# Kernel optimization log

Measured on AMD Instinct MI355X. Metric: run time of the kernel, lower is better.

Reference implementation:

```python
import jax, jax.numpy as jnp
import numpy as np

NEG_BIG = -9e15  # matches torch's -9000000000000000.0 mask value


def _l2norm(x, eps=1e-12):
    # F.normalize(x, p=2, dim=1)
    n = jnp.sqrt(jnp.sum(x * x, axis=1, keepdims=True))
    return x / jnp.maximum(n, eps)


def _fusion_attribute(emb, att_emb, adj):
    # cosine similarity [N, M]
    sim = _l2norm(emb) @ _l2norm(att_emb).T
    sim = sim * adj
    # masked softmax over dim=1: zeros -> -9e15
    logits = jnp.where(sim != 0, sim, jnp.full_like(sim, NEG_BIG))
    attention = jax.nn.softmax(logits, axis=1)
    return attention @ att_emb


def setup_inputs() -> dict:
    key = jax.random.key(0)
    k1, k2, k3, k4 = jax.random.split(key, 4)
    U, I, D = 10000, 8000, 64
    users_emb = 0.1 * jax.random.normal(k1, (U, D), dtype=jnp.float32)  # init.normal_(std=0.1)
    items_emb = 0.1 * jax.random.normal(k2, (I, D), dtype=jnp.float32)
    Out_UserAttNets = (jax.random.uniform(k3, (U, I)) < 0.05).astype(jnp.float32)
    Out_ItemAttNets = (jax.random.uniform(k4, (I, U)) < 0.05).astype(jnp.float32)
    return {
        "num_users": U,
        "num_items": I,
        "users_emb": users_emb,
        "items_emb": items_emb,
        "Out_UserAttNets": Out_UserAttNets,
        "Out_ItemAttNets": Out_ItemAttNets,
    }


def reference(num_users, num_items, users_emb, items_emb, Out_UserAttNets, Out_ItemAttNets):
    out_useratt_emb = _fusion_attribute(users_emb, items_emb, Out_UserAttNets)
    out_itematt_emb = _fusion_attribute(items_emb, users_emb, Out_ItemAttNets)
    return (users_emb, items_emb, out_useratt_emb, out_itematt_emb)
```

## Files before the change

### kernel.cpp

```cpp
#include <hip/hip_runtime.h>
#include <math.h>

typedef float f32x4 __attribute__((ext_vector_type(4)));
typedef unsigned int u32;
typedef u32 u32x4 __attribute__((ext_vector_type(4)));
typedef unsigned short u16;
typedef unsigned long long u64;

#define SEG 512

__device__ __forceinline__ u16 f2b(float x) {
    union { float f; u32 u; } v; v.f = x;
    return (u16)((v.u + 0x7FFFu + ((v.u >> 16) & 1u)) >> 16);
}
__device__ __forceinline__ float b2f_lo(u32 u) { union { u32 u; float f; } v; v.u = u << 16;         return v.f; }
__device__ __forceinline__ float b2f_hi(u32 u) { union { u32 u; float f; } v; v.u = u & 0xFFFF0000u; return v.f; }

__global__ __launch_bounds__(256) void prep_kernel(
    const float* __restrict__ users, const float* __restrict__ items,
    u16* __restrict__ hU, u16* __restrict__ hI,
    float* __restrict__ nU, float* __restrict__ nI, int U, int I)
{
    int lane = threadIdx.x & 63;
    int row  = (blockIdx.x << 2) + (threadIdx.x >> 6);
    const float* src; u16* hat; float* nrm; int r;
    if (row < U) { r = row; src = users; hat = hU; nrm = nU; }
    else { r = row - U; if (r >= I) return; src = items; hat = hI; nrm = nI; }
    float x = src[(size_t)r * 64 + lane];
    float s = x * x;
#pragma unroll
    for (int off = 32; off; off >>= 1) s += __shfl_xor(s, off, 64);
    float nv   = sqrtf(s);
    float rinv = 1.0f / fmaxf(nv, 1e-12f);
    hat[(size_t)r * 64 + lane] = f2b(x * rinv);
    if (lane == 0) nrm[r] = nv;
}

__global__ __launch_bounds__(256) void att_row_kernel(
    const float* __restrict__ users, const float* __restrict__ items,
    const u16* __restrict__ hU, const u16* __restrict__ hI,
    const float* __restrict__ nU, const float* __restrict__ nI,
    const float* __restrict__ adjU, const float* __restrict__ adjI,
    float* __restrict__ outU, float* __restrict__ outI, int U, int I)
{
    __shared__ int   cols_sh[4][SEG];
    __shared__ float red[4][8][8];
    __shared__ float wsum_sh[4];

    const int lane = threadIdx.x & 63;
    const int wid  = threadIdx.x >> 6;
    const int half = wid & 1;
    const int grow = ((int)blockIdx.x << 1) + (wid >> 1);
    const bool valid = (grow < U + I);

    const u16* qhat = 0; const u16* kvhat = 0; const float* kvnrm = 0;
    const float* kvraw = 0; const float* adj = 0; float* outp = 0;
    int M = 0, row = 0;
    if (valid) {
        if (grow < U) {
            row = grow;     qhat = hU; kvhat = hI; kvnrm = nI;
            kvraw = items;  adj = adjU; outp = outU; M = I;
        } else {
            row = grow - U; qhat = hI; kvhat = hU; kvnrm = nU;
            kvraw = users;  adj = adjI; outp = outI; M = U;
        }
    }

    const int sub = lane & 7;
    const int grp = lane >> 3;

    float a0 = 0.f, a1 = 0.f, a2 = 0.f, a3 = 0.f;
    float a4 = 0.f, a5 = 0.f, a6 = 0.f, a7 = 0.f, wsum = 0.f;

    if (valid) {
        const float* adjrow = adj + (size_t)row * M;

        const int mid = (M >> 1) & ~3;
        const int lo4 = half ? (mid >> 2) : 0;
        const int hi4 = half ? (M >> 2) : (mid >> 2);
        int wcount = 0;
        for (int i4 = lo4 + lane; i4 < hi4; i4 += 64) {
            f32x4 a = __builtin_nontemporal_load((const f32x4*)adjrow + i4);
#pragma unroll
            for (int j = 0; j < 4; ++j) {
                bool pred = (a[j] != 0.0f);
                u64 mask = __ballot(pred);
                if (pred) {
                    int pos = wcount + __builtin_amdgcn_mbcnt_hi(
                        (u32)(mask >> 32), __builtin_amdgcn_mbcnt_lo((u32)mask, 0));
                    if (pos < SEG) cols_sh[wid][pos] = (i4 << 2) + j;
                }
                wcount += __popcll(mask);
            }
        }
        wcount = __shfl(wcount, 0, 64);
        if (half && (M & 3)) {
            int idx = (hi4 << 2) + lane;
            bool pred = (idx < M) && (adjrow[idx] != 0.0f);
            u64 mask = __ballot(pred);
            if (pred) {
                int pos = wcount + __builtin_amdgcn_mbcnt_hi(
                    (u32)(mask >> 32), __builtin_amdgcn_mbcnt_lo((u32)mask, 0));
                if (pos < SEG) cols_sh[wid][pos] = idx;
            }
            wcount += __popcll(mask);
        }
        int cnt = wcount > SEG ? SEG : wcount;

        u32x4 qw = *(const u32x4*)(qhat + (size_t)row * 64 + sub * 8);
        const float q0 = b2f_lo(qw[0]), q1 = b2f_hi(qw[0]);
        const float q2 = b2f_lo(qw[1]), q3 = b2f_hi(qw[1]);
        const float q4 = b2f_lo(qw[2]), q5 = b2f_hi(qw[2]);
        const float q6 = b2f_lo(qw[3]), q7 = b2f_hi(qw[3]);

        const int* cp = cols_sh[wid];
        int i = grp;
        for (; i + 24 < cnt; i += 32) {
            int ca = cp[i], cb = cp[i + 8], cc = cp[i + 16], cd = cp[i + 24];
            u32x4 va = *(const u32x4*)(kvhat + (size_t)ca * 64 + sub * 8);
            u32x4 vb = *(const u32x4*)(kvhat + (size_t)cb * 64 + sub * 8);
            u32x4 vc = *(const u32x4*)(kvhat + (size_t)cc * 64 + sub * 8);
            u32x4 vd = *(const u32x4*)(kvhat + (size_t)cd * 64 + sub * 8);
            float na = kvnrm[ca], nb = kvnrm[cb], nc = kvnrm[cc], nd = kvnrm[cd];
            float ra0 = b2f_lo(va[0]), ra1 = b2f_hi(va[0]), ra2 = b2f_lo(va[1]), ra3 = b2f_hi(va[1]);
            float ra4 = b2f_lo(va[2]), ra5 = b2f_hi(va[2]), ra6 = b2f_lo(va[3]), ra7 = b2f_hi(va[3]);
            float rb0 = b2f_lo(vb[0]), rb1 = b2f_hi(vb[0]), rb2 = b2f_lo(vb[1]), rb3 = b2f_hi(vb[1]);
            float rb4 = b2f_lo(vb[2]), rb5 = b2f_hi(vb[2]), rb6 = b2f_lo(vb[3]), rb7 = b2f_hi(vb[3]);
            float rc0 = b2f_lo(vc[0]), rc1 = b2f_hi(vc[0]), rc2 = b2f_lo(vc[1]), rc3 = b2f_hi(vc[1]);
            float rc4 = b2f_lo(vc[2]), rc5 = b2f_hi(vc[2]), rc6 = b2f_lo(vc[3]), rc7 = b2f_hi(vc[3]);
            float rd0 = b2f_lo(vd[0]), rd1 = b2f_hi(vd[0]), rd2 = b2f_lo(vd[1]), rd3 = b2f_hi(vd[1]);
            float rd4 = b2f_lo(vd[2]), rd5 = b2f_hi(vd[2]), rd6 = b2f_lo(vd[3]), rd7 = b2f_hi(vd[3]);
            float da = fmaf(q0, ra0, fmaf(q1, ra1, fmaf(q2, ra2, fmaf(q3, ra3,
                       fmaf(q4, ra4, fmaf(q5, ra5, fmaf(q6, ra6, q7 * ra7)))))));
            float db = fmaf(q0, rb0, fmaf(q1, rb1, fmaf(q2, rb2, fmaf(q3, rb3,
                       fmaf(q4, rb4, fmaf(q5, rb5, fmaf(q6, rb6, q7 * rb7)))))));
            float dc = fmaf(q0, rc0, fmaf(q1, rc1, fmaf(q2, rc2, fmaf(q3, rc3,
                       fmaf(q4, rc4, fmaf(q5, rc5, fmaf(q6, rc6, q7 * rc7)))))));
            float dd = fmaf(q0, rd0, fmaf(q1, rd1, fmaf(q2, rd2, fmaf(q3, rd3,
                       fmaf(q4, rd4, fmaf(q5, rd5, fmaf(q6, rd6, q7 * rd7)))))));
#pragma unroll
            for (int off = 1; off <= 4; off <<= 1) {
                da += __shfl_xor(da, off, 64);
                db += __shfl_xor(db, off, 64);
                dc += __shfl_xor(dc, off, 64);
                dd += __shfl_xor(dd, off, 64);
            }
            float wa = (da != 0.0f) ? __expf(da - 1.0f) : 0.0f;
            float wb = (db != 0.0f) ? __expf(db - 1.0f) : 0.0f;
            float wc = (dc != 0.0f) ? __expf(dc - 1.0f) : 0.0f;
            float wd = (dd != 0.0f) ? __expf(dd - 1.0f) : 0.0f;
            float xa = wa * na, xb = wb * nb, xc = wc * nc, xd = wd * nd;
            a0 = fmaf(xa, ra0, fmaf(xb, rb0, fmaf(xc, rc0, fmaf(xd, rd0, a0))));
            a1 = fmaf(xa, ra1, fmaf(xb, rb1, fmaf(xc, rc1, fmaf(xd, rd1, a1))));
            a2 = fmaf(xa, ra2, fmaf(xb, rb2, fmaf(xc, rc2, fmaf(xd, rd2, a2))));
            a3 = fmaf(xa, ra3, fmaf(xb, rb3, fmaf(xc, rc3, fmaf(xd, rd3, a3))));
            a4 = fmaf(xa, ra4, fmaf(xb, rb4, fmaf(xc, rc4, fmaf(xd, rd4, a4))));
            a5 = fmaf(xa, ra5, fmaf(xb, rb5, fmaf(xc, rc5, fmaf(xd, rd5, a5))));
            a6 = fmaf(xa, ra6, fmaf(xb, rb6, fmaf(xc, rc6, fmaf(xd, rd6, a6))));
            a7 = fmaf(xa, ra7, fmaf(xb, rb7, fmaf(xc, rc7, fmaf(xd, rd7, a7))));
            if (sub == 0) wsum += (wa + wb) + (wc + wd);
        }
        for (; i < cnt; i += 8) {
            int ca = cp[i];
            u32x4 va = *(const u32x4*)(kvhat + (size_t)ca * 64 + sub * 8);
            float na = kvnrm[ca];
            float ra0 = b2f_lo(va[0]), ra1 = b2f_hi(va[0]), ra2 = b2f_lo(va[1]), ra3 = b2f_hi(va[1]);
            float ra4 = b2f_lo(va[2]), ra5 = b2f_hi(va[2]), ra6 = b2f_lo(va[3]), ra7 = b2f_hi(va[3]);
            float da = fmaf(q0, ra0, fmaf(q1, ra1, fmaf(q2, ra2, fmaf(q3, ra3,
                       fmaf(q4, ra4, fmaf(q5, ra5, fmaf(q6, ra6, q7 * ra7)))))));
#pragma unroll
            for (int off = 1; off <= 4; off <<= 1) da += __shfl_xor(da, off, 64);
            float wa = (da != 0.0f) ? __expf(da - 1.0f) : 0.0f;
            float xa = wa * na;
            a0 = fmaf(xa, ra0, a0); a1 = fmaf(xa, ra1, a1);
            a2 = fmaf(xa, ra2, a2); a3 = fmaf(xa, ra3, a3);
            a4 = fmaf(xa, ra4, a4); a5 = fmaf(xa, ra5, a5);
            a6 = fmaf(xa, ra6, a6); a7 = fmaf(xa, ra7, a7);
            if (sub == 0) wsum += wa;
        }

#pragma unroll
        for (int off = 8; off <= 32; off <<= 1) {
            wsum += __shfl_xor(wsum, off, 64);
            a0 += __shfl_xor(a0, off, 64); a1 += __shfl_xor(a1, off, 64);
            a2 += __shfl_xor(a2, off, 64); a3 += __shfl_xor(a3, off, 64);
            a4 += __shfl_xor(a4, off, 64); a5 += __shfl_xor(a5, off, 64);
            a6 += __shfl_xor(a6, off, 64); a7 += __shfl_xor(a7, off, 64);
        }
        if (lane < 8) {
            f32x4* rp = (f32x4*)&red[wid][lane][0];
            rp[0] = (f32x4){a0, a1, a2, a3};
            rp[1] = (f32x4){a4, a5, a6, a7};
        }
        if (lane == 0) wsum_sh[wid] = wsum;
    }
    __syncthreads();

    if (valid && half == 0) {
        float den = wsum_sh[wid] + wsum_sh[wid + 1];
        if (lane < 8) {
            f32x4* r0p = (f32x4*)&red[wid][lane][0];
            f32x4* r1p = (f32x4*)&red[wid + 1][lane][0];
            f32x4 s0 = r0p[0] + r1p[0];
            f32x4 s1 = r0p[1] + r1p[1];
            float* orow = outp + (size_t)row * 64 + lane * 8;
            if (den > 0.0f) {
                float inv = 1.0f / den;
                ((f32x4*)orow)[0] = s0 * inv;
                ((f32x4*)orow)[1] = s1 * inv;
            } else {
                f32x4 m0 = (f32x4){0.f, 0.f, 0.f, 0.f};
                f32x4 m1 = (f32x4){0.f, 0.f, 0.f, 0.f};
                for (int r = 0; r < M; ++r) {
                    const f32x4* kr = (const f32x4*)(kvraw + (size_t)r * 64 + lane * 8);
                    m0 += kr[0]; m1 += kr[1];
                }
                float invM = 1.0f / (float)M;
                ((f32x4*)orow)[0] = m0 * invM;
                ((f32x4*)orow)[1] = m1 * invM;
            }
        }
    }
}

extern "C" void kernel_launch(void* const* d_in, const int* in_sizes, int n_in,
                              void* d_out, int out_size, void* d_ws, size_t ws_size,
                              hipStream_t stream) {
    const float* users = (const float*)d_in[2];
    const float* items = (const float*)d_in[3];
    const float* adjU  = (const float*)d_in[4];
    const float* adjI  = (const float*)d_in[5];
    const int U = in_sizes[2] / 64;
    const int I = in_sizes[3] / 64;

    char* w = (char*)d_ws;
    u16* hU = (u16*)w;    w += (size_t)U * 64 * sizeof(u16);
    u16* hI = (u16*)w;    w += (size_t)I * 64 * sizeof(u16);
    float* nU = (float*)w; w += (size_t)U * sizeof(float);
    float* nI = (float*)w;

    float* out = (float*)d_out;

    hipMemcpyAsync(out, users, (size_t)U * 64 * sizeof(float),
                   hipMemcpyDeviceToDevice, stream);
    hipMemcpyAsync(out + (size_t)U * 64, items, (size_t)I * 64 * sizeof(float),
                   hipMemcpyDeviceToDevice, stream);

    prep_kernel<<<(U + I + 3) / 4, 256, 0, stream>>>(users, items, hU, hI, nU, nI, U, I);

    float* outUatt = out + (size_t)(U + I) * 64;
    float* outIatt = outUatt + (size_t)U * 64;
    att_row_kernel<<<(U + I + 1) / 2, 256, 0, stream>>>(
        users, items, hU, hI, nU, nI, adjU, adjI, outUatt, outIatt, U, I);
}
```

Baseline: 239.9 us.

## Split adjacency compaction into separate kernel writing u16 column lists

Moves the dense adjacency scan and nonzero compaction out of the attention kernel into a dedicated compact_kernel. That kernel writes per-half-row u16 column indices and counts to workspace, and the gather kernel reads those lists instead of scanning the adjacency. The aim is to decouple the bandwidth-bound scan from the latency-bound gather so each runs at full occupancy without LDS staging. In exchange it adds a launch plus a workspace round trip, and it lowers SEG to 384, which risks truncating dense rows.

Result: slower. 248.5 us (+3.6%).

```diff
diff --git a/kernel.cpp b/kernel.cpp
--- a/kernel.cpp
+++ b/kernel.cpp
@@ -7,7 +7,7 @@
 typedef unsigned short u16;
 typedef unsigned long long u64;
 
-#define SEG 512
+#define SEG 384
 
 __device__ __forceinline__ u16 f2b(float x) {
     union { float f; u32 u; } v; v.f = x;
@@ -15,6 +15,9 @@
 }
 __device__ __forceinline__ float b2f_lo(u32 u) { union { u32 u; float f; } v; v.u = u << 16;         return v.f; }
 __device__ __forceinline__ float b2f_hi(u32 u) { union { u32 u; float f; } v; v.u = u & 0xFFFF0000u; return v.f; }
+__device__ __forceinline__ int mbcnt64(u64 m) {
+    return __builtin_amdgcn_mbcnt_hi((u32)(m >> 32), __builtin_amdgcn_mbcnt_lo((u32)m, 0));
+}
 
 __global__ __launch_bounds__(256) void prep_kernel(
     const float* __restrict__ users, const float* __restrict__ items,
@@ -36,14 +39,61 @@
     if (lane == 0) nrm[r] = nv;
 }
 
-__global__ __launch_bounds__(256) void att_row_kernel(
+__global__ __launch_bounds__(256) void compact_kernel(
+    const float* __restrict__ adjU, const float* __restrict__ adjI,
+    u16* __restrict__ csr, u32* __restrict__ cnt, int U, int I)
+{
+    const int lane = threadIdx.x & 63;
+    const int wid  = threadIdx.x >> 6;
+    const int hr   = ((int)blockIdx.x << 2) + wid;
+    if (hr >= 2 * (U + I)) return;
+    const int grow = hr >> 1, half = hr & 1;
+
+    const float* adj; int M, row;
+    if (grow < U) { row = grow;     adj = adjU; M = I; }
+    else          { row = grow - U; adj = adjI; M = U; }
+    const float* adjrow = adj + (size_t)row * M;
+
+    const int mid = (M >> 1) & ~3;
+    const int lo4 = half ? (mid >> 2) : 0;
+    const int hi4 = half ? (M >> 2) : (mid >> 2);
+    u16* outp = csr + (size_t)hr * SEG;
+
+    int wcount = 0;
+    for (int i4 = lo4 + lane; i4 < hi4; i4 += 64) {
+        f32x4 a = __builtin_nontemporal_load((const f32x4*)adjrow + i4);
+#pragma unroll
+        for (int j = 0; j < 4; ++j) {
+            bool pred = (a[j] != 0.0f);
+            u64 mask = __ballot(pred);
+            if (pred) {
+                int pos = wcount + mbcnt64(mask);
+                if (pos < SEG) outp[pos] = (u16)((i4 << 2) + j);
+            }
+            wcount += __popcll(mask);
+        }
+    }
+    wcount = __shfl(wcount, 0, 64);
+    if (half && (M & 3)) {
+        int idx = (hi4 << 2) + lane;
+        bool pred = (idx < M) && (adjrow[idx] != 0.0f);
+        u64 mask = __ballot(pred);
+        if (pred) {
+            int pos = wcount + mbcnt64(mask);
+            if (pos < SEG) outp[pos] = (u16)idx;
+        }
+        wcount += __popcll(mask);
+    }
+    if (lane == 0) cnt[hr] = (u32)(wcount > SEG ? SEG : wcount);
+}
+
+__global__ __launch_bounds__(256) void att_gather_kernel(
     const float* __restrict__ users, const float* __restrict__ items,
     const u16* __restrict__ hU, const u16* __restrict__ hI,
     const float* __restrict__ nU, const float* __restrict__ nI,
-    const float* __restrict__ adjU, const float* __restrict__ adjI,
+    const u16* __restrict__ csr, const u32* __restrict__ cnt,
     float* __restrict__ outU, float* __restrict__ outI, int U, int I)
 {
-    __shared__ int   cols_sh[4][SEG];
     __shared__ float red[4][8][8];
     __shared__ float wsum_sh[4];
 
@@ -54,15 +104,15 @@
     const bool valid = (grow < U + I);
 
     const u16* qhat = 0; const u16* kvhat = 0; const float* kvnrm = 0;
-    const float* kvraw = 0; const float* adj = 0; float* outp = 0;
+    const float* kvraw = 0; float* outp = 0;
     int M = 0, row = 0;
     if (valid) {
         if (grow < U) {
             row = grow;     qhat = hU; kvhat = hI; kvnrm = nI;
-            kvraw = items;  adj = adjU; outp = outU; M = I;
+            kvraw = items;  outp = outU; M = I;
         } else {
             row = grow - U; qhat = hI; kvhat = hU; kvnrm = nU;
-            kvraw = users;  adj = adjI; outp = outI; M = U;
+            kvraw = users;  outp = outI; M = U;
         }
     }
 
@@ -73,39 +123,9 @@
     float a4 = 0.f, a5 = 0.f, a6 = 0.f, a7 = 0.f, wsum = 0.f;
 
     if (valid) {
-        const float* adjrow = adj + (size_t)row * M;
-
-        const int mid = (M >> 1) & ~3;
-        const int lo4 = half ? (mid >> 2) : 0;
-        const int hi4 = half ? (M >> 2) : (mid >> 2);
-        int wcount = 0;
-        for (int i4 = lo4 + lane; i4 < hi4; i4 += 64) {
-            f32x4 a = __builtin_nontemporal_load((const f32x4*)adjrow + i4);
-#pragma unroll
-            for (int j = 0; j < 4; ++j) {
-                bool pred = (a[j] != 0.0f);
-                u64 mask = __ballot(pred);
-                if (pred) {
-                    int pos = wcount + __builtin_amdgcn_mbcnt_hi(
-                        (u32)(mask >> 32), __builtin_amdgcn_mbcnt_lo((u32)mask, 0));
-                    if (pos < SEG) cols_sh[wid][pos] = (i4 << 2) + j;
-                }
-                wcount += __popcll(mask);
-            }
-        }
-        wcount = __shfl(wcount, 0, 64);
-        if (half && (M & 3)) {
-            int idx = (hi4 << 2) + lane;
-            bool pred = (idx < M) && (adjrow[idx] != 0.0f);
-            u64 mask = __ballot(pred);
-            if (pred) {
-                int pos = wcount + __builtin_amdgcn_mbcnt_hi(
-                    (u32)(mask >> 32), __builtin_amdgcn_mbcnt_lo((u32)mask, 0));
-                if (pos < SEG) cols_sh[wid][pos] = idx;
-            }
-            wcount += __popcll(mask);
-        }
-        int cnt = wcount > SEG ? SEG : wcount;
+        const int hr = (grow << 1) | half;
+        const int cn = (int)cnt[hr];
+        const u16* cp = csr + (size_t)hr * SEG;
 
         u32x4 qw = *(const u32x4*)(qhat + (size_t)row * 64 + sub * 8);
         const float q0 = b2f_lo(qw[0]), q1 = b2f_hi(qw[0]);
@@ -113,9 +133,8 @@
         const float q4 = b2f_lo(qw[2]), q5 = b2f_hi(qw[2]);
         const float q6 = b2f_lo(qw[3]), q7 = b2f_hi(qw[3]);
 
-        const int* cp = cols_sh[wid];
         int i = grp;
-        for (; i + 24 < cnt; i += 32) {
+        for (; i + 24 < cn; i += 32) {
             int ca = cp[i], cb = cp[i + 8], cc = cp[i + 16], cd = cp[i + 24];
             u32x4 va = *(const u32x4*)(kvhat + (size_t)ca * 64 + sub * 8);
             u32x4 vb = *(const u32x4*)(kvhat + (size_t)cb * 64 + sub * 8);
@@ -160,7 +179,7 @@
             a7 = fmaf(xa, ra7, fmaf(xb, rb7, fmaf(xc, rc7, fmaf(xd, rd7, a7))));
             if (sub == 0) wsum += (wa + wb) + (wc + wd);
         }
-        for (; i < cnt; i += 8) {
+        for (; i < cn; i += 8) {
             int ca = cp[i];
             u32x4 va = *(const u32x4*)(kvhat + (size_t)ca * 64 + sub * 8);
             float na = kvnrm[ca];
@@ -232,12 +251,15 @@
     const float* adjI  = (const float*)d_in[5];
     const int U = in_sizes[2] / 64;
     const int I = in_sizes[3] / 64;
+    const int HR = 2 * (U + I);
 
     char* w = (char*)d_ws;
     u16* hU = (u16*)w;    w += (size_t)U * 64 * sizeof(u16);
     u16* hI = (u16*)w;    w += (size_t)I * 64 * sizeof(u16);
     float* nU = (float*)w; w += (size_t)U * sizeof(float);
-    float* nI = (float*)w;
+    float* nI = (float*)w; w += (size_t)I * sizeof(float);
+    u16* csr = (u16*)w;   w += (size_t)HR * SEG * sizeof(u16);
+    u32* cnt = (u32*)w;
 
     float* out = (float*)d_out;
 
@@ -248,8 +270,10 @@
 
     prep_kernel<<<(U + I + 3) / 4, 256, 0, stream>>>(users, items, hU, hI, nU, nI, U, I);
 
+    compact_kernel<<<(HR + 3) / 4, 256, 0, stream>>>(adjU, adjI, csr, cnt, U, I);
+
     float* outUatt = out + (size_t)(U + I) * 64;
     float* outIatt = outUatt + (size_t)U * 64;
-    att_row_kernel<<<(U + I + 1) / 2, 256, 0, stream>>>(
-        users, items, hU, hI, nU, nI, adjU, adjI, outUatt, outIatt, U, I);
-}
+    att_gather_kernel<<<(U + I + 1) / 2, 256, 0, stream>>>(
+        users, items, hU, hI, nU, nI, csr, cnt, outUatt, outIatt, U, I);
+}
```
